# Performance work log

Hardware: AMD Instinct MI355X
Metric: run time of the kernel (lower is better)

The kernel has to match this reference:

```python
import jax, jax.numpy as jnp
import numpy as np

TAU = 0.5
EPS_NORM = 1e-12  # torch F.normalize eps
EPS_DEN = 1e-8


def setup_inputs() -> dict:
    key = jax.random.key(0)
    k1, k2 = jax.random.split(key)
    N, D = 16384, 128
    z1 = jax.random.normal(k1, (N, D), dtype=jnp.float32)
    z2 = jax.random.normal(k2, (N, D), dtype=jnp.float32)
    return {"z1": z1, "z2": z2}


def _l2norm(x):
    # torch F.normalize: x / max(||x||, eps)
    n = jnp.sqrt(jnp.sum(x * x, axis=-1, keepdims=True))
    return x / jnp.maximum(n, EPS_NORM)


def reference(z1, z2):
    z1n = _l2norm(z1)
    z2n = _l2norm(z2)
    # cosine similarity of unit vectors == dot product -> single GEMM [N, N]
    sim = jnp.exp(jnp.einsum('id,jd->ij', z1n, z2n) / TAU)
    pos = jnp.exp(jnp.sum(z1n * z2n, axis=-1) / TAU)  # diagonal positives [N]
    denom = jnp.sum(sim, axis=1) + EPS_DEN
    loss = -jnp.mean(jnp.log(pos / denom))
    return loss
```

## Files before the change

### kernel.cpp

```cpp
#include <hip/hip_runtime.h>
#include <hip/hip_bf16.h>
#include <hip/hip_fp8.h>


#define N_ROWS 16384
#define DIM 128
#define JSPLIT 16
#define COLS_PER_BLOCK (N_ROWS / JSPLIT)
#define JCHUNK 32
#define NCHUNK (COLS_PER_BLOCK / JCHUNK)
#define ROWS_PER_BLOCK 128
#define ITILES (N_ROWS / ROWS_PER_BLOCK)
#define GRID_TOTAL (ITILES * JSPLIT)

#define SCALE 2.8853900817779268f

typedef __attribute__((ext_vector_type(8))) int   int8v;
typedef __attribute__((ext_vector_type(4))) int   int4v;
typedef __attribute__((ext_vector_type(4))) float floatx4;

#if __has_builtin(__builtin_amdgcn_exp2f)
#define EXP2(x) __builtin_amdgcn_exp2f(x)
#else
#define EXP2(x) exp2f(x)
#endif

__device__ inline floatx4 mfma_fp8_k128(int8v a, int8v b, floatx4 c) {
  return __builtin_amdgcn_mfma_scale_f32_16x16x128_f8f6f4(
      a, b, c, 0, 0, 0, 0x7F7F7F7F, 0, 0x7F7F7F7F);
}

__device__ inline void gload_lds16(const void* gptr, void* lptr) {
  __builtin_amdgcn_global_load_lds(
      (const __attribute__((address_space(1))) void*)gptr,
      (__attribute__((address_space(3))) void*)lptr, 16, 0, 0);
}

__device__ inline short pack_fp8x2(float x, float y) {
#if __has_builtin(__builtin_amdgcn_cvt_pk_fp8_f32)
  int p = __builtin_amdgcn_cvt_pk_fp8_f32(x, y, 0, false);
  return (short)(p & 0xFFFF);
#else
  __hip_fp8_e4m3 a(x), b(y);
  return (short)((unsigned char)a.__x | ((unsigned short)(unsigned char)b.__x << 8));
#endif
}

__global__ __launch_bounds__(256) void norm_kernel(
    const float* __restrict__ z1, const float* __restrict__ z2,
    unsigned char* __restrict__ z1q, unsigned char* __restrict__ z2q,
    float* __restrict__ diag, float* __restrict__ denom,
    float* __restrict__ out) {
  int tid = threadIdx.x;
  int wave = tid >> 6, lane = tid & 63;
  int row = blockIdx.x * 4 + wave;
  const float2* p1 = (const float2*)(z1 + (size_t)row * DIM);
  const float2* p2 = (const float2*)(z2 + (size_t)row * DIM);
  float2 a = p1[lane], b = p2[lane];
  float s11 = a.x * a.x + a.y * a.y;
  float s22 = b.x * b.x + b.y * b.y;
  float s12 = a.x * b.x + a.y * b.y;
#pragma unroll
  for (int m = 32; m >= 1; m >>= 1) {
    s11 += __shfl_xor(s11, m);
    s22 += __shfl_xor(s22, m);
    s12 += __shfl_xor(s12, m);
  }
  float inv1 = 1.0f / fmaxf(sqrtf(s11), 1e-12f);
  float inv2 = 1.0f / fmaxf(sqrtf(s22), 1e-12f);
  float sc1 = inv1 * SCALE;
  ((short*)(z1q + (size_t)row * DIM))[lane] = pack_fp8x2(a.x * sc1, a.y * sc1);
  ((short*)(z2q + (size_t)row * DIM))[lane] = pack_fp8x2(b.x * inv2, b.y * inv2);
  if (lane == 0) {
    diag[row]  = s12 * inv1 * inv2;
    denom[row] = 0.0f;
  }
  if (blockIdx.x == 0 && tid == 0) out[0] = 0.0f;
}

__global__ __launch_bounds__(256, 4) void sim_kernel(
    const unsigned char* __restrict__ z1q,
    const unsigned char* __restrict__ z2q,
    float* __restrict__ denom) {
  __shared__ int4v lds[2][JCHUNK * 8];

  int tid = threadIdx.x;
  int w   = tid >> 6;
  int q   = (tid >> 4) & 3;
  int l15 = tid & 15;
  int s   = l15 & 7;
  int itile  = blockIdx.x & (ITILES - 1);
  int jsplit = blockIdx.x >> 7;
  int i0 = itile * ROWS_PER_BLOCK + w * 32;

  const floatx4 ZERO4 = {0.f, 0.f, 0.f, 0.f};

  int8v afrag[2];
#pragma unroll
  for (int ii = 0; ii < 2; ++ii) {
    const int4v* rp = (const int4v*)(z1q + (size_t)(i0 + ii * 16 + l15) * DIM);
    int4v a0 = rp[q * 2], a1 = rp[q * 2 + 1];
    int8v af;
    af[0] = a0[0]; af[1] = a0[1]; af[2] = a0[2]; af[3] = a0[3];
    af[4] = a1[0]; af[5] = a1[1]; af[6] = a1[2]; af[7] = a1[3];
    afrag[ii] = af;
  }

  floatx4 rowsum[2];
  rowsum[0] = ZERO4;
  rowsum[1] = ZERO4;
  floatx4 pacc0 = {-1e30f, -1e30f, -1e30f, -1e30f};
  floatx4 pacc1 = {-1e30f, -1e30f, -1e30f, -1e30f};

  const char* Bbase = (const char*)z2q + (size_t)jsplit * COLS_PER_BLOCK * DIM;

#define STAGE(cidx, bufi)                                                    \
  do {                                                                       \
    const char* _ck = Bbase + (size_t)(cidx) * JCHUNK * DIM;                 \
    char* _dst = (char*)&lds[bufi][0];                                       \
    int _row = tid >> 3, _gl = tid & 7;                                      \
    int _u = _gl ^ (_row & 7);                                               \
    int _o = 2 * (_u & 3) + (_u >> 2);                                       \
    gload_lds16(_ck + (size_t)_row * DIM + _o * 16,                          \
                _dst + (size_t)tid * 16);                                    \
  } while (0)

  STAGE(0, 0);
  __syncthreads();

  int lo_i = q ^ s;
  int hi_i = lo_i ^ 4;

  for (int c = 0; c < NCHUNK; ++c) {
    if (c + 1 < NCHUNK) STAGE(c + 1, (c + 1) & 1);
    const int4v* buf = &lds[c & 1][0];

#pragma unroll
    for (int jj = 0; jj < 2; ++jj) {
      int rbase = (jj * 16 + l15) * 8;
      int4v lo = buf[rbase + lo_i];
      int4v hi = buf[rbase + hi_i];
      int8v bf;
      bf[0] = lo[0]; bf[1] = lo[1]; bf[2] = lo[2]; bf[3] = lo[3];
      bf[4] = hi[0]; bf[5] = hi[1]; bf[6] = hi[2]; bf[7] = hi[3];

      {
        floatx4 nacc = mfma_fp8_k128(afrag[0], bf, ZERO4);
        floatx4 e;
#pragma unroll
        for (int r = 0; r < 4; ++r) e[r] = EXP2(pacc0[r]);
        rowsum[0] += e;
        pacc0 = nacc;
      }
      {
        floatx4 nacc = mfma_fp8_k128(afrag[1], bf, ZERO4);
        floatx4 e;
#pragma unroll
        for (int r = 0; r < 4; ++r) e[r] = EXP2(pacc1[r]);
        rowsum[1] += e;
        pacc1 = nacc;
      }
    }
    __syncthreads();
  }
  {
    floatx4 e;
#pragma unroll
    for (int r = 0; r < 4; ++r) e[r] = EXP2(pacc0[r]);
    rowsum[0] += e;
#pragma unroll
    for (int r = 0; r < 4; ++r) e[r] = EXP2(pacc1[r]);
    rowsum[1] += e;
  }

#pragma unroll
  for (int ii = 0; ii < 2; ++ii)
#pragma unroll
    for (int r = 0; r < 4; ++r) {
      float v = rowsum[ii][r];
      v += __shfl_xor(v, 1);
      v += __shfl_xor(v, 2);
      v += __shfl_xor(v, 4);
      v += __shfl_xor(v, 8);
      if (l15 == 0) atomicAdd(&denom[i0 + ii * 16 + q * 4 + r], v);
    }
}

__global__ __launch_bounds__(256) void loss_kernel(
    const float* __restrict__ denom, const float* __restrict__ diag,
    float* __restrict__ out) {
  int row = blockIdx.x * 256 + threadIdx.x;
  float t = 2.0f * diag[row] - __logf(denom[row] + 1e-8f);
#pragma unroll
  for (int m = 32; m >= 1; m >>= 1) t += __shfl_xor(t, m);
  if ((threadIdx.x & 63) == 0) atomicAdd(out, -t * (1.0f / N_ROWS));
}

extern "C" void kernel_launch(void* const* d_in, const int* in_sizes, int n_in,
                              void* d_out, int out_size, void* d_ws, size_t ws_size,
                              hipStream_t stream) {
  const float* z1 = (const float*)d_in[0];
  const float* z2 = (const float*)d_in[1];
  char* ws = (char*)d_ws;
  unsigned char* z1q = (unsigned char*)ws;
  unsigned char* z2q = (unsigned char*)(ws + (size_t)N_ROWS * DIM);
  float* denom = (float*)(ws + (size_t)2 * N_ROWS * DIM);
  float* diag  = (float*)(ws + (size_t)2 * N_ROWS * DIM + (size_t)N_ROWS * 4);
  float* outp  = (float*)d_out;

  norm_kernel<<<N_ROWS / 4, 256, 0, stream>>>(z1, z2, z1q, z2q, diag, denom, outp);
  sim_kernel<<<GRID_TOTAL, 256, 0, stream>>>(z1q, z2q, denom);
  loss_kernel<<<N_ROWS / 256, 256, 0, stream>>>(denom, diag, outp);
}
```

Before: 110.7 us.

## Deepen LDS staging to four buffers with prefetch distance two and explicit waitcnts

Turns the double-buffered global-to-LDS staging of z2 chunks into a four-slot ring that prefetches two chunks ahead. The full __syncthreads is replaced by manual s_waitcnt vmcnt(1)/lgkmcnt(0) plus a raw s_barrier, so one load can stay in flight across each barrier. Address arithmetic is hoisted out of the loop and the loop is unrolled by four. This is meant to hide global load latency behind MFMA/exp work, at the cost of more LDS per block and relying on hand-written waitcnt correctness.

```diff
diff --git a/kernel.cpp b/kernel.cpp
--- a/kernel.cpp
+++ b/kernel.cpp
@@ -12,6 +12,8 @@
 #define ROWS_PER_BLOCK 128
 #define ITILES (N_ROWS / ROWS_PER_BLOCK)
 #define GRID_TOTAL (ITILES * JSPLIT)
+#define CHUNK_BYTES (JCHUNK * DIM)
+#define BUF_BYTES (JCHUNK * 8 * 16)
 
 #define SCALE 2.8853900817779268f
 
@@ -82,7 +84,7 @@
     const unsigned char* __restrict__ z1q,
     const unsigned char* __restrict__ z2q,
     float* __restrict__ denom) {
-  __shared__ int4v lds[2][JCHUNK * 8];
+  __shared__ int4v lds[4][JCHUNK * 8];
 
   int tid = threadIdx.x;
   int w   = tid >> 6;
@@ -114,26 +116,28 @@
 
   const char* Bbase = (const char*)z2q + (size_t)jsplit * COLS_PER_BLOCK * DIM;
 
-#define STAGE(cidx, bufi)                                                    \
-  do {                                                                       \
-    const char* _ck = Bbase + (size_t)(cidx) * JCHUNK * DIM;                 \
-    char* _dst = (char*)&lds[bufi][0];                                       \
-    int _row = tid >> 3, _gl = tid & 7;                                      \
-    int _u = _gl ^ (_row & 7);                                               \
-    int _o = 2 * (_u & 3) + (_u >> 2);                                       \
-    gload_lds16(_ck + (size_t)_row * DIM + _o * 16,                          \
-                _dst + (size_t)tid * 16);                                    \
-  } while (0)
+  int _row = tid >> 3, _gl = tid & 7;
+  int _u = _gl ^ (_row & 7);
+  int _o = 2 * (_u & 3) + (_u >> 2);
+  const char* gsrc = Bbase + (size_t)_row * DIM + _o * 16;
+  char* ldst = (char*)&lds[0][0] + (size_t)tid * 16;
+
+#define STAGE(cidx, bufi)                                                     \
+  gload_lds16(gsrc + (size_t)(cidx) * CHUNK_BYTES,                            \
+              ldst + (size_t)(bufi) * BUF_BYTES)
 
   STAGE(0, 0);
-  __syncthreads();
+  STAGE(1, 1);
+  asm volatile("s_waitcnt vmcnt(1)" ::: "memory");
+  __builtin_amdgcn_s_barrier();
 
   int lo_i = q ^ s;
   int hi_i = lo_i ^ 4;
 
+#pragma unroll 4
   for (int c = 0; c < NCHUNK; ++c) {
-    if (c + 1 < NCHUNK) STAGE(c + 1, (c + 1) & 1);
-    const int4v* buf = &lds[c & 1][0];
+    if (c + 2 < NCHUNK) STAGE(c + 2, (c + 2) & 3);
+    const int4v* buf = &lds[c & 3][0];
 
 #pragma unroll
     for (int jj = 0; jj < 2; ++jj) {
@@ -161,7 +165,14 @@
         pacc1 = nacc;
       }
     }
-    __syncthreads();
+
+    if (c + 1 < NCHUNK) {
+      if (c + 2 < NCHUNK)
+        asm volatile("s_waitcnt vmcnt(1) lgkmcnt(0)" ::: "memory");
+      else
+        asm volatile("s_waitcnt vmcnt(0) lgkmcnt(0)" ::: "memory");
+      __builtin_amdgcn_s_barrier();
+    }
   }
   {
     floatx4 e;
```

Result: no change. 111.2 us (+0.5%).

## Load B fragments directly from global memory instead of LDS staging

Applied to the files above, without the earlier changes.

Drops the double-buffered LDS staging of z2q chunks (global_load_lds plus barriers). Each lane now reads its 32-byte B fragment straight from global memory, relying on L1/L2 since all four waves read the same columns. Occupancy hint rises from 4 to 8 blocks per CU and the chunk loop is kept rolled. This removes barrier and LDS traffic, at the cost of redundant global/L1 loads per wave and no explicit prefetch to hide latency.

```diff
diff --git a/kernel.cpp b/kernel.cpp
--- a/kernel.cpp
+++ b/kernel.cpp
@@ -28,12 +28,6 @@
 __device__ inline floatx4 mfma_fp8_k128(int8v a, int8v b, floatx4 c) {
   return __builtin_amdgcn_mfma_scale_f32_16x16x128_f8f6f4(
       a, b, c, 0, 0, 0, 0x7F7F7F7F, 0, 0x7F7F7F7F);
-}
-
-__device__ inline void gload_lds16(const void* gptr, void* lptr) {
-  __builtin_amdgcn_global_load_lds(
-      (const __attribute__((address_space(1))) void*)gptr,
-      (__attribute__((address_space(3))) void*)lptr, 16, 0, 0);
 }
 
 __device__ inline short pack_fp8x2(float x, float y) {
@@ -78,17 +72,14 @@
   if (blockIdx.x == 0 && tid == 0) out[0] = 0.0f;
 }
 
-__global__ __launch_bounds__(256, 4) void sim_kernel(
+__global__ __launch_bounds__(256, 8) void sim_kernel(
     const unsigned char* __restrict__ z1q,
     const unsigned char* __restrict__ z2q,
     float* __restrict__ denom) {
-  __shared__ int4v lds[2][JCHUNK * 8];
-
   int tid = threadIdx.x;
   int w   = tid >> 6;
   int q   = (tid >> 4) & 3;
   int l15 = tid & 15;
-  int s   = l15 & 7;
   int itile  = blockIdx.x & (ITILES - 1);
   int jsplit = blockIdx.x >> 7;
   int i0 = itile * ROWS_PER_BLOCK + w * 32;
@@ -112,34 +103,17 @@
   floatx4 pacc0 = {-1e30f, -1e30f, -1e30f, -1e30f};
   floatx4 pacc1 = {-1e30f, -1e30f, -1e30f, -1e30f};
 
-  const char* Bbase = (const char*)z2q + (size_t)jsplit * COLS_PER_BLOCK * DIM;
+  const char* Bbase = (const char*)z2q +
+      (size_t)(jsplit * COLS_PER_BLOCK + l15) * DIM + q * 32;
 
-#define STAGE(cidx, bufi)                                                    \
-  do {                                                                       \
-    const char* _ck = Bbase + (size_t)(cidx) * JCHUNK * DIM;                 \
-    char* _dst = (char*)&lds[bufi][0];                                       \
-    int _row = tid >> 3, _gl = tid & 7;                                      \
-    int _u = _gl ^ (_row & 7);                                               \
-    int _o = 2 * (_u & 3) + (_u >> 2);                                       \
-    gload_lds16(_ck + (size_t)_row * DIM + _o * 16,                          \
-                _dst + (size_t)tid * 16);                                    \
-  } while (0)
-
-  STAGE(0, 0);
-  __syncthreads();
-
-  int lo_i = q ^ s;
-  int hi_i = lo_i ^ 4;
-
+#pragma unroll 1
   for (int c = 0; c < NCHUNK; ++c) {
-    if (c + 1 < NCHUNK) STAGE(c + 1, (c + 1) & 1);
-    const int4v* buf = &lds[c & 1][0];
-
 #pragma unroll
     for (int jj = 0; jj < 2; ++jj) {
-      int rbase = (jj * 16 + l15) * 8;
-      int4v lo = buf[rbase + lo_i];
-      int4v hi = buf[rbase + hi_i];
+      const int4v* rp =
+          (const int4v*)(Bbase + (size_t)(c * JCHUNK + jj * 16) * DIM);
+      int4v lo = rp[0];
+      int4v hi = rp[1];
       int8v bf;
       bf[0] = lo[0]; bf[1] = lo[1]; bf[2] = lo[2]; bf[3] = lo[3];
       bf[4] = hi[0]; bf[5] = hi[1]; bf[6] = hi[2]; bf[7] = hi[3];
@@ -161,7 +135,6 @@
         pacc1 = nacc;
       }
     }
-    __syncthreads();
   }
   {
     floatx4 e;
```

Result: slower. 188.4 us (+70.2%).
